# Performance work log

Hardware: AMD Instinct MI355X
Metric: run time of the kernel (lower is better)

Reference implementation:

```python
import jax, jax.numpy as jnp
import numpy as np

N_USER = 100000
N_ITEM = 50000
D = 128
OUT = 128
E = 1600000


def setup_inputs() -> dict:
    key = jax.random.key(0)
    ks = jax.random.split(key, 8)
    glorot = 1.0 / np.sqrt(D)
    x_user = jax.random.normal(ks[0], (N_USER, D), dtype=jnp.float32)
    x_item = jax.random.normal(ks[1], (N_ITEM, D), dtype=jnp.float32)
    W_ui_src = jax.random.normal(ks[2], (D, OUT), dtype=jnp.float32) * glorot
    W_ui_tgt = jax.random.normal(ks[3], (D, OUT), dtype=jnp.float32) * glorot
    W_iu_src = jax.random.normal(ks[4], (D, OUT), dtype=jnp.float32) * glorot
    W_iu_tgt = jax.random.normal(ks[5], (D, OUT), dtype=jnp.float32) * glorot
    # edge_ui: row 0 = user (source) indices, row 1 = item (target) indices
    edge_ui = jnp.stack([
        jax.random.randint(ks[6], (E,), 0, N_USER),
        jax.random.randint(jax.random.fold_in(ks[6], 1), (E,), 0, N_ITEM),
    ]).astype(jnp.int64)
    # edge_iu: row 0 = item (source) indices, row 1 = user (target) indices
    edge_iu = jnp.stack([
        jax.random.randint(ks[7], (E,), 0, N_ITEM),
        jax.random.randint(jax.random.fold_in(ks[7], 1), (E,), 0, N_USER),
    ]).astype(jnp.int64)
    return {
        "x_user": x_user, "x_item": x_item,
        "W_ui_src": W_ui_src, "W_ui_tgt": W_ui_tgt,
        "W_iu_src": W_iu_src, "W_iu_tgt": W_iu_tgt,
        "edge_ui": edge_ui, "edge_iu": edge_iu,
    }


def _sage_conv(x_src, x_tgt, W_src, W_tgt, edge, n_tgt):
    # per-edge-type linear projections
    src = x_src @ W_src            # [n_src, OUT]
    tgt = x_tgt @ W_tgt            # [n_tgt, OUT]
    # gather projected source features per edge, scatter-mean into targets
    gathered = src[edge[0]]        # [E, OUT]
    seg_sum = jax.ops.segment_sum(gathered, edge[1], num_segments=n_tgt)
    cnt = jax.ops.segment_sum(jnp.ones((edge.shape[1],), src.dtype), edge[1],
                              num_segments=n_tgt)
    mean = seg_sum / jnp.maximum(cnt, 1.0)[:, None]  # zero rows stay zero
    return tgt + mean


def reference(x_user, x_item, W_ui_src, W_ui_tgt, W_iu_src, W_iu_tgt,
              edge_ui, edge_iu):
    # edge type (user -> item): output for node type 'item'
    out_item = _sage_conv(x_user, x_item, W_ui_src, W_ui_tgt, edge_ui,
                          x_item.shape[0])
    # edge type (item -> user): output for node type 'user'
    out_user = _sage_conv(x_item, x_user, W_iu_src, W_iu_tgt, edge_iu,
                          x_user.shape[0])
    return out_user, out_item
```

## Files before the change

### kernel.cpp

```cpp
#include <hip/hip_runtime.h>


#define D_FEAT 128

static constexpr int kNUser = 100000;
static constexpr int kNItem = 50000;
static constexpr int kNTot  = kNItem + kNUser;
static constexpr int kIB    = (kNItem + 255) / 256;
static constexpr int kUB    = (kNUser + 255) / 256;
static constexpr int NBUCK  = kIB + kUB;
static constexpr int CHUNK  = 6250;
static constexpr int NCHUNK = 512;
static constexpr int SEGCAP = 9216;

typedef short bf16x8 __attribute__((ext_vector_type(8)));
typedef float f32x4 __attribute__((ext_vector_type(4)));
typedef float f32x2 __attribute__((ext_vector_type(2)));

__device__ inline unsigned bf16rne(float f) {
  const unsigned u = __float_as_uint(f);
  return (u + 0x7fffu + ((u >> 16) & 1u)) >> 16;
}

__device__ inline int bucket_of(int t) {
  return (t < kNItem) ? (t >> 8) : (kIB + ((t - kNItem) >> 8));
}

__global__ __launch_bounds__(256) void phase_a_kernel(
    const float* __restrict__ xu, const float* __restrict__ xi,
    unsigned short* __restrict__ xbu, unsigned short* __restrict__ xbi,
    unsigned char* __restrict__ xf8u, unsigned char* __restrict__ xf8i,
    const float* __restrict__ Wt0, const float* __restrict__ Ws0,
    const float* __restrict__ Wt1, const float* __restrict__ Ws1,
    unsigned short* __restrict__ bp,
    const int* __restrict__ eui_t, const int* __restrict__ eiu_t,
    unsigned* __restrict__ gh, int n8u, int n8t, int E) {
  __shared__ unsigned lh[NBUCK];
  const int b = (int)blockIdx.x;
  const int tid = (int)threadIdx.x;

  if (b < 2048) {
    for (int i = b * 256 + tid; i < n8t; i += 2048 * 256) {
      const float* in = (i < n8u) ? xu : xi;
      unsigned short* outb = (i < n8u) ? xbu : xbi;
      unsigned char* out8 = (i < n8u) ? xf8u : xf8i;
      const int j = (i < n8u) ? i : (i - n8u);
      const float4 a = ((const float4*)in)[(size_t)j * 2];
      const float4 c = ((const float4*)in)[(size_t)j * 2 + 1];
      uint4 r;
      r.x = bf16rne(a.x) | (bf16rne(a.y) << 16);
      r.y = bf16rne(a.z) | (bf16rne(a.w) << 16);
      r.z = bf16rne(c.x) | (bf16rne(c.y) << 16);
      r.w = bf16rne(c.z) | (bf16rne(c.w) << 16);
      ((uint4*)outb)[j] = r;
      uint2 q;
      q.x = (unsigned)__builtin_amdgcn_cvt_pk_fp8_f32(a.x, a.y, 0, false);
      q.x = (unsigned)__builtin_amdgcn_cvt_pk_fp8_f32(a.z, a.w, (int)q.x, true);
      q.y = (unsigned)__builtin_amdgcn_cvt_pk_fp8_f32(c.x, c.y, 0, false);
      q.y = (unsigned)__builtin_amdgcn_cvt_pk_fp8_f32(c.z, c.w, (int)q.y, true);
      ((uint2*)out8)[j] = q;
    }
  } else if (b < 2080) {
    const int t = (b - 2048) * 256 + tid;
    if (t < 2 * 8 * 8 * 64) {
      const int pair = t >> 12;
      const int kk = (t >> 9) & 7;
      const int n = (t >> 6) & 7;
      const int l = t & 63;
      const int c = n * 16 + (l & 15);
      const int k0 = kk * 32 + (l >> 4) * 8;
      const float* Wt = pair ? Wt1 : Wt0;
      const float* Ws = pair ? Ws1 : Ws0;
      unsigned v[8];
#pragma unroll
      for (int j = 0; j < 8; ++j) {
        const int k = k0 + j;
        const float f = (k < 128) ? Wt[k * 128 + c] : Ws[(k - 128) * 128 + c];
        v[j] = bf16rne(f);
      }
      uint4 r;
      r.x = v[0] | (v[1] << 16);
      r.y = v[2] | (v[3] << 16);
      r.z = v[4] | (v[5] << 16);
      r.w = v[6] | (v[7] << 16);
      ((uint4*)bp)[t] = r;
    }
  } else {
    for (int k = tid; k < NBUCK; k += 256) lh[k] = 0;
    __syncthreads();
    const int total = 2 * E;
    const int beg = (b - 2080) * CHUNK;
    const int end = min(beg + CHUNK, total);
    for (int i = beg + tid; i < end; i += 256) {
      const int t = (i < E) ? eui_t[i] : (eiu_t[i - E] + kNItem);
      atomicAdd(&lh[bucket_of(t)], 1u);
    }
    __syncthreads();
    for (int k = tid; k < NBUCK; k += 256)
      if (lh[k]) atomicAdd(&gh[k], lh[k]);
  }
}

__global__ __launch_bounds__(256) void p2_scan_kernel(
    const unsigned* __restrict__ gh, unsigned* __restrict__ bstart,
    unsigned* __restrict__ gcur) {
  __shared__ unsigned ts[256];
  const int tid = threadIdx.x;
  unsigned v[4];
  unsigned tsum = 0;
#pragma unroll
  for (int i = 0; i < 4; ++i) {
    const int idx = tid * 4 + i;
    v[i] = (idx < NBUCK) ? gh[idx] : 0u;
    tsum += v[i];
  }
  ts[tid] = tsum;
  __syncthreads();
  unsigned x = tsum;
  for (int off = 1; off < 256; off <<= 1) {
    const unsigned y = (tid >= off) ? ts[tid - off] : 0u;
    __syncthreads();
    x += y;
    ts[tid] = x;
    __syncthreads();
  }
  unsigned run = x - tsum;
#pragma unroll
  for (int i = 0; i < 4; ++i) {
    const int idx = tid * 4 + i;
    if (idx < NBUCK) { bstart[idx] = run; gcur[idx] = run; }
    run += v[i];
  }
  if (tid == 255) bstart[NBUCK] = run;
}

__global__ __launch_bounds__(256) void p3_partition_kernel(
    const int* __restrict__ eui_s, const int* __restrict__ eui_t,
    const int* __restrict__ eiu_s, const int* __restrict__ eiu_t,
    unsigned* __restrict__ gcur, unsigned* __restrict__ part, int E) {
  __shared__ unsigned lh[NBUCK], lbase[NBUCK], lcur[NBUCK], lpref[NBUCK];
  __shared__ unsigned ts[256];
  __shared__ unsigned lstage[CHUNK];
  __shared__ unsigned short lbuck[CHUNK];
  const int tid = (int)threadIdx.x;
  for (int k = tid; k < NBUCK; k += 256) { lh[k] = 0; lcur[k] = 0; }
  __syncthreads();

  const int total = 2 * E;
  const int beg = (int)blockIdx.x * CHUNK;
  const int end = min(beg + CHUNK, total);
  const int csz = end - beg;

  for (int i = beg + tid; i < end; i += 256) {
    const int t = (i < E) ? eui_t[i] : (eiu_t[i - E] + kNItem);
    atomicAdd(&lh[bucket_of(t)], 1u);
  }
  __syncthreads();

  for (int k = tid; k < NBUCK; k += 256)
    lbase[k] = lh[k] ? atomicAdd(&gcur[k], lh[k]) : 0u;
  {
    unsigned v[3];
    unsigned tsum = 0;
#pragma unroll
    for (int i = 0; i < 3; ++i) {
      const int idx = tid * 3 + i;
      v[i] = (idx < NBUCK) ? lh[idx] : 0u;
      tsum += v[i];
    }
    ts[tid] = tsum;
    __syncthreads();
    unsigned x = tsum;
    for (int off = 1; off < 256; off <<= 1) {
      const unsigned y = (tid >= off) ? ts[tid - off] : 0u;
      __syncthreads();
      x += y;
      ts[tid] = x;
      __syncthreads();
    }
    unsigned run = x - tsum;
#pragma unroll
    for (int i = 0; i < 3; ++i) {
      const int idx = tid * 3 + i;
      if (idx < NBUCK) lpref[idx] = run;
      run += v[i];
    }
  }
  __syncthreads();

  for (int i = beg + tid; i < end; i += 256) {
    int s, t;
    if (i < E) { s = eui_s[i]; t = eui_t[i]; }
    else       { s = eiu_s[i - E]; t = eiu_t[i - E] + kNItem; }
    const int k = bucket_of(t);
    const unsigned tl = (t < kNItem) ? (unsigned)(t & 255) : (unsigned)((t - kNItem) & 255);
    const unsigned r = atomicAdd(&lcur[k], 1u);
    const unsigned idx = lpref[k] + r;
    lstage[idx] = (unsigned)s | (tl << 24);
    lbuck[idx] = (unsigned short)k;
  }
  __syncthreads();

  for (int j = tid; j < csz; j += 256) {
    const int k = lbuck[j];
    part[lbase[k] + (j - lpref[k])] = lstage[j];
  }
}

__global__ __launch_bounds__(256) void p4_csr_kernel(
    const unsigned* __restrict__ part, const unsigned* __restrict__ bstart,
    unsigned* __restrict__ csr, unsigned* __restrict__ offs,
    unsigned* __restrict__ cnt) {
  __shared__ unsigned lcnt[256], lofs[256], lcur[256], ts[256];
  __shared__ unsigned segbuf[SEGCAP];
  const int k = (int)blockIdx.x;
  const int tid = (int)threadIdx.x;
  const unsigned seg0 = bstart[k], seg1 = bstart[k + 1];
  const int tbase = (k < kIB) ? (k << 8) : (kNItem + ((k - kIB) << 8));
  const int tmax = (k < kIB) ? min(256, kNItem - tbase) : min(256, kNTot - tbase);

  lcnt[tid] = 0;
  __syncthreads();
  for (unsigned i = seg0 + tid; i < seg1; i += 256)
    atomicAdd(&lcnt[part[i] >> 24], 1u);
  __syncthreads();

  const unsigned v = lcnt[tid];
  ts[tid] = v;
  __syncthreads();
  unsigned x = v;
  for (int off = 1; off < 256; off <<= 1) {
    const unsigned y = (tid >= off) ? ts[tid - off] : 0u;
    __syncthreads();
    x += y;
    ts[tid] = x;
    __syncthreads();
  }
  lofs[tid] = x - v;
  lcur[tid] = 0;
  if (tid < tmax) { offs[tbase + tid] = seg0 + (x - v); cnt[tbase + tid] = v; }
  __syncthreads();

  for (unsigned i = seg0 + tid; i < seg1; i += 256) {
    const unsigned e = part[i];
    const unsigned tl = e >> 24;
    const unsigned r = atomicAdd(&lcur[tl], 1u);
    const unsigned slot = lofs[tl] + r;
    if (slot < SEGCAP) segbuf[slot] = e & 0x00FFFFFFu;
  }
  __syncthreads();

  const unsigned segsz = min(seg1 - seg0, (unsigned)SEGCAP);
  for (unsigned j = tid; j < segsz; j += 256) csr[seg0 + j] = segbuf[j];
}

__global__ __launch_bounds__(256) void aggregate2_kernel(
    const unsigned char* __restrict__ xf8u, const unsigned char* __restrict__ xf8i,
    const unsigned* __restrict__ csr, const unsigned* __restrict__ offs,
    const unsigned* __restrict__ cnt, unsigned short* __restrict__ meanb) {
  const int lane = (int)(threadIdx.x & 63);
  const int sub = lane >> 4;
  const unsigned sl8 = (unsigned)(lane & 15) * 8u;
  const int node = (int)((blockIdx.x * 256 + threadIdx.x) >> 6);
  if (node >= kNTot) return;
  const unsigned char* xf = (node < kNItem) ? xf8u : xf8i;
  const unsigned deg = cnt[node];
  const unsigned start = offs[node];
  const unsigned end = start + deg;

  f32x2 a0 = {0.f, 0.f}, a1 = {0.f, 0.f}, a2 = {0.f, 0.f}, a3 = {0.f, 0.f};

  unsigned base = start;
  for (; base + 16 <= end; base += 16) {
    const unsigned s0 = csr[base + sub];
    const unsigned s1 = csr[base + sub + 4];
    const unsigned s2 = csr[base + sub + 8];
    const unsigned s3 = csr[base + sub + 12];
    const uint2 v0 = *(const uint2*)(xf + (size_t)(s0 * 128u + sl8));
    const uint2 v1 = *(const uint2*)(xf + (size_t)(s1 * 128u + sl8));
    const uint2 v2 = *(const uint2*)(xf + (size_t)(s2 * 128u + sl8));
    const uint2 v3 = *(const uint2*)(xf + (size_t)(s3 * 128u + sl8));
#pragma unroll
    for (int h = 0; h < 4; ++h) {
      const uint2 v = (h == 0) ? v0 : (h == 1) ? v1 : (h == 2) ? v2 : v3;
      a0 += __builtin_amdgcn_cvt_pk_f32_fp8((int)v.x, false);
      a1 += __builtin_amdgcn_cvt_pk_f32_fp8((int)v.x, true);
      a2 += __builtin_amdgcn_cvt_pk_f32_fp8((int)v.y, false);
      a3 += __builtin_amdgcn_cvt_pk_f32_fp8((int)v.y, true);
    }
  }
  if (base < end) {
    const unsigned i0 = base + sub;
    const unsigned i1 = i0 + 4;
    const unsigned i2 = i0 + 8;
    const unsigned i3 = i0 + 12;
    uint2 v0 = make_uint2(0, 0), v1 = make_uint2(0, 0);
    uint2 v2 = make_uint2(0, 0), v3 = make_uint2(0, 0);
    if (i0 < end) v0 = *(const uint2*)(xf + (size_t)(csr[i0] * 128u + sl8));
    if (i1 < end) v1 = *(const uint2*)(xf + (size_t)(csr[i1] * 128u + sl8));
    if (i2 < end) v2 = *(const uint2*)(xf + (size_t)(csr[i2] * 128u + sl8));
    if (i3 < end) v3 = *(const uint2*)(xf + (size_t)(csr[i3] * 128u + sl8));
#pragma unroll
    for (int h = 0; h < 4; ++h) {
      const uint2 v = (h == 0) ? v0 : (h == 1) ? v1 : (h == 2) ? v2 : v3;
      a0 += __builtin_amdgcn_cvt_pk_f32_fp8((int)v.x, false);
      a1 += __builtin_amdgcn_cvt_pk_f32_fp8((int)v.x, true);
      a2 += __builtin_amdgcn_cvt_pk_f32_fp8((int)v.y, false);
      a3 += __builtin_amdgcn_cvt_pk_f32_fp8((int)v.y, true);
    }
  }

  float acc[8] = {a0.x, a0.y, a1.x, a1.y, a2.x, a2.y, a3.x, a3.y};
#pragma unroll
  for (int j = 0; j < 8; ++j) acc[j] += __shfl_xor(acc[j], 16);
#pragma unroll
  for (int j = 0; j < 8; ++j) acc[j] += __shfl_xor(acc[j], 32);

  if (sub == 0) {
    const float inv = deg ? 1.0f / (float)deg : 0.0f;
    uint4 r;
    r.x = bf16rne(acc[0] * inv) | (bf16rne(acc[1] * inv) << 16);
    r.y = bf16rne(acc[2] * inv) | (bf16rne(acc[3] * inv) << 16);
    r.z = bf16rne(acc[4] * inv) | (bf16rne(acc[5] * inv) << 16);
    r.w = bf16rne(acc[6] * inv) | (bf16rne(acc[7] * inv) << 16);
    *(uint4*)(meanb + (size_t)node * D_FEAT + sl8) = r;
  }
}

__global__ __launch_bounds__(256) void mfma_out2_kernel(
    const unsigned short* __restrict__ xbi, const unsigned short* __restrict__ xbu,
    const unsigned short* __restrict__ meanb,
    const unsigned short* __restrict__ bpack,
    float* __restrict__ out_user, float* __restrict__ out_item, int itemBlocks) {
  const int b = (int)blockIdx.x;
  const unsigned short *xb, *mb, *bp;
  float* out;
  int M, rowb;
  if (b < itemBlocks) {
    M = kNItem; rowb = b * 64;
    xb = xbi; mb = meanb; out = out_item; bp = bpack;
  } else {
    M = kNUser; rowb = (b - itemBlocks) * 64;
    xb = xbu; mb = meanb + (size_t)kNItem * D_FEAT; out = out_user;
    bp = bpack + (size_t)8 * 8 * 64 * 8;
  }
  const int l = (int)(threadIdx.x & 63);
  const int w = (int)(threadIdx.x >> 6);
  rowb += w * 16;
  const int arow = min(rowb + (l & 15), M - 1);
  const int kq8 = (l >> 4) * 8;

  f32x4 acc[8];
#pragma unroll
  for (int n = 0; n < 8; ++n) acc[n] = (f32x4){0.f, 0.f, 0.f, 0.f};

  const unsigned short* ax = xb + (size_t)arow * D_FEAT + kq8;
  const unsigned short* am = mb + (size_t)arow * D_FEAT + kq8;

#pragma unroll
  for (int kk = 0; kk < 8; ++kk) {
    const unsigned short* ap = (kk < 4) ? (ax + kk * 32) : (am + (kk - 4) * 32);
    const bf16x8 a = *(const bf16x8*)ap;
#pragma unroll
    for (int n = 0; n < 8; ++n) {
      const bf16x8 bfr = *(const bf16x8*)(bp + ((size_t)(kk * 8 + n) * 64 + l) * 8);
      acc[n] = __builtin_amdgcn_mfma_f32_16x16x32_bf16(a, bfr, acc[n], 0, 0, 0);
    }
  }

  const int r0 = rowb + (l >> 4) * 4;
  const int col = l & 15;
#pragma unroll
  for (int n = 0; n < 8; ++n) {
#pragma unroll
    for (int r = 0; r < 4; ++r) {
      const int row = r0 + r;
      if (row < M) out[(size_t)row * 128 + n * 16 + col] = acc[n][r];
    }
  }
}

extern "C" void kernel_launch(void* const* d_in, const int* in_sizes, int n_in,
                              void* d_out, int out_size, void* d_ws, size_t ws_size,
                              hipStream_t stream) {
  const float* x_user  = (const float*)d_in[0];
  const float* x_item  = (const float*)d_in[1];
  const float* W_ui_src = (const float*)d_in[2];
  const float* W_ui_tgt = (const float*)d_in[3];
  const float* W_iu_src = (const float*)d_in[4];
  const float* W_iu_tgt = (const float*)d_in[5];
  const int* edge_ui = (const int*)d_in[6];
  const int* edge_iu = (const int*)d_in[7];
  const int E = in_sizes[6] / 2;

  unsigned short* meanb = (unsigned short*)d_ws;
  unsigned short* xbu   = meanb + (size_t)kNTot * 128;
  unsigned short* xbi   = xbu + (size_t)kNUser * 128;
  unsigned short* bpack = xbi + (size_t)kNItem * 128;
  unsigned* gh     = (unsigned*)(bpack + 2 * 256 * 128);
  unsigned* bstart = gh + NBUCK;
  unsigned* gcur   = bstart + (NBUCK + 1);
  unsigned* cnt    = gcur + NBUCK;
  unsigned* offs   = cnt + kNTot;

  float* out_user = (float*)d_out;
  float* out_item = out_user + (size_t)kNUser * 128;

  unsigned* csr = (unsigned*)d_out;
  unsigned* part = csr + (size_t)2 * E;
  unsigned char* xf8u = (unsigned char*)(part + (size_t)2 * E);
  unsigned char* xf8i = xf8u + (size_t)kNUser * 128;

  hipMemsetAsync(gh, 0, NBUCK * sizeof(unsigned), stream);

  phase_a_kernel<<<2048 + 32 + NCHUNK, 256, 0, stream>>>(
      x_user, x_item, xbu, xbi, xf8u, xf8i,
      W_ui_tgt, W_ui_src, W_iu_tgt, W_iu_src, bpack,
      edge_ui + E, edge_iu + E, gh,
      kNUser * 128 / 8, kNTot * 128 / 8, E);

  p2_scan_kernel<<<1, 256, 0, stream>>>(gh, bstart, gcur);
  p3_partition_kernel<<<NCHUNK, 256, 0, stream>>>(
      edge_ui, edge_ui + E, edge_iu, edge_iu + E, gcur, part, E);
  p4_csr_kernel<<<NBUCK, 256, 0, stream>>>(part, bstart, csr, offs, cnt);

  aggregate2_kernel<<<(kNTot * 64 + 255) / 256, 256, 0, stream>>>(
      xf8u, xf8i, csr, offs, cnt, meanb);

  const int itemBlocks = (kNItem + 63) / 64;
  const int userBlocks = (kNUser + 63) / 64;
  mfma_out2_kernel<<<itemBlocks + userBlocks, 256, 0, stream>>>(
      xbi, xbu, meanb, bpack, out_user, out_item, itemBlocks);
}
```

Baseline: 208.1 us.

## Fuse neighbor mean aggregation into MFMA output kernel via LDS

```diff
diff --git a/kernel.cpp b/kernel.cpp
--- a/kernel.cpp
+++ b/kernel.cpp
@@ -254,99 +254,101 @@
   for (unsigned j = tid; j < segsz; j += 256) csr[seg0 + j] = segbuf[j];
 }
 
-__global__ __launch_bounds__(256) void aggregate2_kernel(
+__global__ __launch_bounds__(256) void agg_mfma_kernel(
     const unsigned char* __restrict__ xf8u, const unsigned char* __restrict__ xf8i,
+    const unsigned short* __restrict__ xbi, const unsigned short* __restrict__ xbu,
     const unsigned* __restrict__ csr, const unsigned* __restrict__ offs,
-    const unsigned* __restrict__ cnt, unsigned short* __restrict__ meanb) {
-  const int lane = (int)(threadIdx.x & 63);
-  const int sub = lane >> 4;
-  const unsigned sl8 = (unsigned)(lane & 15) * 8u;
-  const int node = (int)((blockIdx.x * 256 + threadIdx.x) >> 6);
-  if (node >= kNTot) return;
-  const unsigned char* xf = (node < kNItem) ? xf8u : xf8i;
-  const unsigned deg = cnt[node];
-  const unsigned start = offs[node];
-  const unsigned end = start + deg;
-
-  f32x2 a0 = {0.f, 0.f}, a1 = {0.f, 0.f}, a2 = {0.f, 0.f}, a3 = {0.f, 0.f};
-
-  unsigned base = start;
-  for (; base + 16 <= end; base += 16) {
-    const unsigned s0 = csr[base + sub];
-    const unsigned s1 = csr[base + sub + 4];
-    const unsigned s2 = csr[base + sub + 8];
-    const unsigned s3 = csr[base + sub + 12];
-    const uint2 v0 = *(const uint2*)(xf + (size_t)(s0 * 128u + sl8));
-    const uint2 v1 = *(const uint2*)(xf + (size_t)(s1 * 128u + sl8));
-    const uint2 v2 = *(const uint2*)(xf + (size_t)(s2 * 128u + sl8));
-    const uint2 v3 = *(const uint2*)(xf + (size_t)(s3 * 128u + sl8));
-#pragma unroll
-    for (int h = 0; h < 4; ++h) {
-      const uint2 v = (h == 0) ? v0 : (h == 1) ? v1 : (h == 2) ? v2 : v3;
-      a0 += __builtin_amdgcn_cvt_pk_f32_fp8((int)v.x, false);
-      a1 += __builtin_amdgcn_cvt_pk_f32_fp8((int)v.x, true);
-      a2 += __builtin_amdgcn_cvt_pk_f32_fp8((int)v.y, false);
-      a3 += __builtin_amdgcn_cvt_pk_f32_fp8((int)v.y, true);
-    }
-  }
-  if (base < end) {
-    const unsigned i0 = base + sub;
-    const unsigned i1 = i0 + 4;
-    const unsigned i2 = i0 + 8;
-    const unsigned i3 = i0 + 12;
-    uint2 v0 = make_uint2(0, 0), v1 = make_uint2(0, 0);
-    uint2 v2 = make_uint2(0, 0), v3 = make_uint2(0, 0);
-    if (i0 < end) v0 = *(const uint2*)(xf + (size_t)(csr[i0] * 128u + sl8));
-    if (i1 < end) v1 = *(const uint2*)(xf + (size_t)(csr[i1] * 128u + sl8));
-    if (i2 < end) v2 = *(const uint2*)(xf + (size_t)(csr[i2] * 128u + sl8));
-    if (i3 < end) v3 = *(const uint2*)(xf + (size_t)(csr[i3] * 128u + sl8));
-#pragma unroll
-    for (int h = 0; h < 4; ++h) {
-      const uint2 v = (h == 0) ? v0 : (h == 1) ? v1 : (h == 2) ? v2 : v3;
-      a0 += __builtin_amdgcn_cvt_pk_f32_fp8((int)v.x, false);
-      a1 += __builtin_amdgcn_cvt_pk_f32_fp8((int)v.x, true);
-      a2 += __builtin_amdgcn_cvt_pk_f32_fp8((int)v.y, false);
-      a3 += __builtin_amdgcn_cvt_pk_f32_fp8((int)v.y, true);
-    }
-  }
-
-  float acc[8] = {a0.x, a0.y, a1.x, a1.y, a2.x, a2.y, a3.x, a3.y};
-#pragma unroll
-  for (int j = 0; j < 8; ++j) acc[j] += __shfl_xor(acc[j], 16);
-#pragma unroll
-  for (int j = 0; j < 8; ++j) acc[j] += __shfl_xor(acc[j], 32);
-
-  if (sub == 0) {
-    const float inv = deg ? 1.0f / (float)deg : 0.0f;
-    uint4 r;
-    r.x = bf16rne(acc[0] * inv) | (bf16rne(acc[1] * inv) << 16);
-    r.y = bf16rne(acc[2] * inv) | (bf16rne(acc[3] * inv) << 16);
-    r.z = bf16rne(acc[4] * inv) | (bf16rne(acc[5] * inv) << 16);
-    r.w = bf16rne(acc[6] * inv) | (bf16rne(acc[7] * inv) << 16);
-    *(uint4*)(meanb + (size_t)node * D_FEAT + sl8) = r;
-  }
-}
-
-__global__ __launch_bounds__(256) void mfma_out2_kernel(
-    const unsigned short* __restrict__ xbi, const unsigned short* __restrict__ xbu,
-    const unsigned short* __restrict__ meanb,
-    const unsigned short* __restrict__ bpack,
+    const unsigned* __restrict__ cnt, const unsigned short* __restrict__ bpack,
     float* __restrict__ out_user, float* __restrict__ out_item, int itemBlocks) {
+  __shared__ unsigned short mlds[64][136];
+
   const int b = (int)blockIdx.x;
-  const unsigned short *xb, *mb, *bp;
+  const unsigned char* xf;
+  const unsigned short *xb, *bp;
   float* out;
-  int M, rowb;
+  int M, rowb_blk, cidOff;
   if (b < itemBlocks) {
-    M = kNItem; rowb = b * 64;
-    xb = xbi; mb = meanb; out = out_item; bp = bpack;
+    M = kNItem; rowb_blk = b * 64; cidOff = 0;
+    xf = xf8u; xb = xbi; out = out_item; bp = bpack;
   } else {
-    M = kNUser; rowb = (b - itemBlocks) * 64;
-    xb = xbu; mb = meanb + (size_t)kNItem * D_FEAT; out = out_user;
+    M = kNUser; rowb_blk = (b - itemBlocks) * 64; cidOff = kNItem;
+    xf = xf8i; xb = xbu; out = out_user;
     bp = bpack + (size_t)8 * 8 * 64 * 8;
   }
+
   const int l = (int)(threadIdx.x & 63);
   const int w = (int)(threadIdx.x >> 6);
-  rowb += w * 16;
+  const int sub = l >> 4;
+  const unsigned sl8 = (unsigned)(l & 15) * 8u;
+
+#pragma unroll 1
+  for (int i = 0; i < 16; ++i) {
+    const int r = w * 16 + i;
+    const int nl = min(rowb_blk + r, M - 1);
+    const int cid = cidOff + nl;
+    const unsigned deg = cnt[cid];
+    const unsigned start = offs[cid];
+    const unsigned end = start + deg;
+
+    f32x2 a0 = {0.f, 0.f}, a1 = {0.f, 0.f}, a2 = {0.f, 0.f}, a3 = {0.f, 0.f};
+    unsigned base = start;
+    for (; base + 16 <= end; base += 16) {
+      const unsigned s0 = csr[base + sub];
+      const unsigned s1 = csr[base + sub + 4];
+      const unsigned s2 = csr[base + sub + 8];
+      const unsigned s3 = csr[base + sub + 12];
+      const uint2 v0 = *(const uint2*)(xf + (size_t)(s0 * 128u + sl8));
+      const uint2 v1 = *(const uint2*)(xf + (size_t)(s1 * 128u + sl8));
+      const uint2 v2 = *(const uint2*)(xf + (size_t)(s2 * 128u + sl8));
+      const uint2 v3 = *(const uint2*)(xf + (size_t)(s3 * 128u + sl8));
+#pragma unroll
+      for (int h = 0; h < 4; ++h) {
+        const uint2 v = (h == 0) ? v0 : (h == 1) ? v1 : (h == 2) ? v2 : v3;
+        a0 += __builtin_amdgcn_cvt_pk_f32_fp8((int)v.x, false);
+        a1 += __builtin_amdgcn_cvt_pk_f32_fp8((int)v.x, true);
+        a2 += __builtin_amdgcn_cvt_pk_f32_fp8((int)v.y, false);
+        a3 += __builtin_amdgcn_cvt_pk_f32_fp8((int)v.y, true);
+      }
+    }
+    if (base < end) {
+      const unsigned i0 = base + sub;
+      const unsigned i1 = i0 + 4;
+      const unsigned i2 = i0 + 8;
+      const unsigned i3 = i0 + 12;
+      uint2 v0 = make_uint2(0, 0), v1 = make_uint2(0, 0);
+      uint2 v2 = make_uint2(0, 0), v3 = make_uint2(0, 0);
+      if (i0 < end) v0 = *(const uint2*)(xf + (size_t)(csr[i0] * 128u + sl8));
+      if (i1 < end) v1 = *(const uint2*)(xf + (size_t)(csr[i1] * 128u + sl8));
+      if (i2 < end) v2 = *(const uint2*)(xf + (size_t)(csr[i2] * 128u + sl8));
+      if (i3 < end) v3 = *(const uint2*)(xf + (size_t)(csr[i3] * 128u + sl8));
+#pragma unroll
+      for (int h = 0; h < 4; ++h) {
+        const uint2 v = (h == 0) ? v0 : (h == 1) ? v1 : (h == 2) ? v2 : v3;
+        a0 += __builtin_amdgcn_cvt_pk_f32_fp8((int)v.x, false);
+        a1 += __builtin_amdgcn_cvt_pk_f32_fp8((int)v.x, true);
+        a2 += __builtin_amdgcn_cvt_pk_f32_fp8((int)v.y, false);
+        a3 += __builtin_amdgcn_cvt_pk_f32_fp8((int)v.y, true);
+      }
+    }
+
+    float acc[8] = {a0.x, a0.y, a1.x, a1.y, a2.x, a2.y, a3.x, a3.y};
+#pragma unroll
+    for (int j = 0; j < 8; ++j) acc[j] += __shfl_xor(acc[j], 16);
+#pragma unroll
+    for (int j = 0; j < 8; ++j) acc[j] += __shfl_xor(acc[j], 32);
+
+    if (sub == 0) {
+      const float inv = deg ? 1.0f / (float)deg : 0.0f;
+      uint4 rr;
+      rr.x = bf16rne(acc[0] * inv) | (bf16rne(acc[1] * inv) << 16);
+      rr.y = bf16rne(acc[2] * inv) | (bf16rne(acc[3] * inv) << 16);
+      rr.z = bf16rne(acc[4] * inv) | (bf16rne(acc[5] * inv) << 16);
+      rr.w = bf16rne(acc[6] * inv) | (bf16rne(acc[7] * inv) << 16);
+      *(uint4*)&mlds[r][(l & 15) * 8] = rr;
+    }
+  }
+
+  const int rowb = rowb_blk + w * 16;
   const int arow = min(rowb + (l & 15), M - 1);
   const int kq8 = (l >> 4) * 8;
 
@@ -355,12 +357,20 @@
   for (int n = 0; n < 8; ++n) acc[n] = (f32x4){0.f, 0.f, 0.f, 0.f};
 
   const unsigned short* ax = xb + (size_t)arow * D_FEAT + kq8;
-  const unsigned short* am = mb + (size_t)arow * D_FEAT + kq8;
-
-#pragma unroll
-  for (int kk = 0; kk < 8; ++kk) {
-    const unsigned short* ap = (kk < 4) ? (ax + kk * 32) : (am + (kk - 4) * 32);
-    const bf16x8 a = *(const bf16x8*)ap;
+
+#pragma unroll
+  for (int kk = 0; kk < 4; ++kk) {
+    const bf16x8 a = *(const bf16x8*)(ax + kk * 32);
+#pragma unroll
+    for (int n = 0; n < 8; ++n) {
+      const bf16x8 bfr = *(const bf16x8*)(bp + ((size_t)(kk * 8 + n) * 64 + l) * 8);
+      acc[n] = __builtin_amdgcn_mfma_f32_16x16x32_bf16(a, bfr, acc[n], 0, 0, 0);
+    }
+  }
+  const unsigned short* aml = &mlds[w * 16 + (l & 15)][kq8];
+#pragma unroll
+  for (int kk = 4; kk < 8; ++kk) {
+    const bf16x8 a = *(const bf16x8*)(aml + (kk - 4) * 32);
 #pragma unroll
     for (int n = 0; n < 8; ++n) {
       const bf16x8 bfr = *(const bf16x8*)(bp + ((size_t)(kk * 8 + n) * 64 + l) * 8);
@@ -393,8 +403,7 @@
   const int* edge_iu = (const int*)d_in[7];
   const int E = in_sizes[6] / 2;
 
-  unsigned short* meanb = (unsigned short*)d_ws;
-  unsigned short* xbu   = meanb + (size_t)kNTot * 128;
+  unsigned short* xbu   = (unsigned short*)d_ws;
   unsigned short* xbi   = xbu + (size_t)kNUser * 128;
   unsigned short* bpack = xbi + (size_t)kNItem * 128;
   unsigned* gh     = (unsigned*)(bpack + 2 * 256 * 128);
@@ -402,14 +411,14 @@
   unsigned* gcur   = bstart + (NBUCK + 1);
   unsigned* cnt    = gcur + NBUCK;
   unsigned* offs   = cnt + kNTot;
+  unsigned* csr    = offs + kNTot;
+  unsigned char* xf8u = (unsigned char*)(csr + (size_t)2 * E);
+  unsigned char* xf8i = xf8u + (size_t)kNUser * 128;
 
   float* out_user = (float*)d_out;
   float* out_item = out_user + (size_t)kNUser * 128;
 
-  unsigned* csr = (unsigned*)d_out;
-  unsigned* part = csr + (size_t)2 * E;
-  unsigned char* xf8u = (unsigned char*)(part + (size_t)2 * E);
-  unsigned char* xf8i = xf8u + (size_t)kNUser * 128;
+  unsigned* part = (unsigned*)d_out;
 
   hipMemsetAsync(gh, 0, NBUCK * sizeof(unsigned), stream);
 
@@ -424,11 +433,9 @@
       edge_ui, edge_ui + E, edge_iu, edge_iu + E, gcur, part, E);
   p4_csr_kernel<<<NBUCK, 256, 0, stream>>>(part, bstart, csr, offs, cnt);
 
-  aggregate2_kernel<<<(kNTot * 64 + 255) / 256, 256, 0, stream>>>(
-      xf8u, xf8i, csr, offs, cnt, meanb);
-
   const int itemBlocks = (kNItem + 63) / 64;
   const int userBlocks = (kNUser + 63) / 64;
-  mfma_out2_kernel<<<itemBlocks + userBlocks, 256, 0, stream>>>(
-      xbi, xbu, meanb, bpack, out_user, out_item, itemBlocks);
-}
+  agg_mfma_kernel<<<itemBlocks + userBlocks, 256, 0, stream>>>(
+      xf8u, xf8i, xbi, xbu, csr, offs, cnt, bpack,
+      out_user, out_item, itemBlocks);
+}
```

Result: slower. 255.2 us (+22.6%).
